# Kernel tuning notes

Hardware: AMD Instinct MI355X
Metric: run time of the kernel (lower is better)

## Reference

```python
import jax, jax.numpy as jnp
import numpy as np

B, N, M, D = 4, 4096, 4096, 64


def setup_inputs() -> dict:
    key = jax.random.key(0)
    kx, ky = jax.random.split(key)
    x = jax.random.normal(kx, (B, N, D), dtype=jnp.float32)
    y = jax.random.normal(ky, (B, M, D), dtype=jnp.float32)
    return {"x": x, "y": y}


def reference(x, y):
    # SparseMatmul3D forward: batched x @ y^T -> [B, N, M]
    return jnp.einsum("bnd,bmd->bnm", x, y)
```

## Files before the change

kernel.cpp:

```cpp
#include <hip/hip_runtime.h>


#define BATCH 4
#define NN 4096
#define MM 4096
#define DD 64

typedef __attribute__((ext_vector_type(8))) short bf16x8;
typedef __attribute__((ext_vector_type(4))) float f32x4;

__device__ __forceinline__ unsigned short f2bf(float f) {
    unsigned u = __builtin_bit_cast(unsigned, f);
    u += 0x7FFFu + ((u >> 16) & 1u);
    return (unsigned short)(u >> 16);
}

__device__ __forceinline__ bf16x8 cvt8(f32x4 v0, f32x4 v1) {
    bf16x8 r;
    r[0] = (short)f2bf(v0[0]); r[1] = (short)f2bf(v0[1]);
    r[2] = (short)f2bf(v0[2]); r[3] = (short)f2bf(v0[3]);
    r[4] = (short)f2bf(v1[0]); r[5] = (short)f2bf(v1[1]);
    r[6] = (short)f2bf(v1[2]); r[7] = (short)f2bf(v1[3]);
    return r;
}

__device__ __forceinline__ void stage_panel(const float* __restrict__ src,
                                            short* __restrict__ dst, int t) {
#pragma unroll
    for (int u = 0; u < 4; ++u) {
        const int f = u * 4096 + t * 8;
        f32x4 v0 = *reinterpret_cast<const f32x4*>(src + f);
        f32x4 v1 = *reinterpret_cast<const f32x4*>(src + f + 4);
        const int r  = (u << 6) + (t >> 3);
        const int un = (t & 7) ^ (r & 7);
        *reinterpret_cast<bf16x8*>(&dst[r * 64 + un * 8]) = cvt8(v0, v1);
    }
}

__global__ __launch_bounds__(512, 4) void
SparseMatmul3D_36155034698289_kernel(const float* __restrict__ x,
                                     const float* __restrict__ y,
                                     float* __restrict__ out) {
    const int bid = blockIdx.x;
    const int mc  = bid & 15;
    const int nt  = (bid >> 4) & 15;
    const int b   = bid >> 8;
    const int n0  = nt * 256;
    const int m0  = mc * 256;

    const int tid   = threadIdx.x;
    const int w     = tid >> 6;
    const int lane  = tid & 63;
    const int row16 = lane & 15;
    const int kgrp  = lane >> 4;
    const int wr    = w >> 1;
    const int wcp   = (w & 1) * 2;
    const int nloc  = wr * 64;

    __shared__ short xs[256 * 64];
    __shared__ short ys[256 * 64];

    stage_panel(x + (size_t)b * NN * DD + (size_t)n0 * DD, xs, tid);
    stage_panel(y + (size_t)b * MM * DD + (size_t)m0 * DD, ys, tid);
    __syncthreads();

    float* __restrict__ ob = out + (size_t)b * NN * MM;

#pragma unroll
    for (int tt = 0; tt < 2; ++tt) {
        const int mloc = (wcp + tt) * 64;

        f32x4 acc[4][4];
#pragma unroll
        for (int i = 0; i < 4; ++i)
#pragma unroll
            for (int j = 0; j < 4; ++j)
                acc[i][j] = (f32x4){0.f, 0.f, 0.f, 0.f};

#pragma unroll
        for (int i = 0; i < 4; ++i) {
            const int ra = mloc + i * 16 + row16;
            const bf16x8 a0 = *reinterpret_cast<const bf16x8*>(
                &ys[ra * 64 + ((kgrp       ^ (ra & 7)) * 8)]);
            const bf16x8 a1 = *reinterpret_cast<const bf16x8*>(
                &ys[ra * 64 + (((4 | kgrp) ^ (ra & 7)) * 8)]);
#pragma unroll
            for (int j = 0; j < 4; ++j) {
                const int rb = nloc + j * 16 + row16;
                const bf16x8 b0 = *reinterpret_cast<const bf16x8*>(
                    &xs[rb * 64 + ((kgrp       ^ (rb & 7)) * 8)]);
                const bf16x8 b1 = *reinterpret_cast<const bf16x8*>(
                    &xs[rb * 64 + (((4 | kgrp) ^ (rb & 7)) * 8)]);
                acc[i][j] = __builtin_amdgcn_mfma_f32_16x16x32_bf16(
                    a0, b0, acc[i][j], 0, 0, 0);
                acc[i][j] = __builtin_amdgcn_mfma_f32_16x16x32_bf16(
                    a1, b1, acc[i][j], 0, 0, 0);
            }
        }

#pragma unroll
        for (int j = 0; j < 4; ++j) {
            float* orow = ob + (size_t)(n0 + nloc + j * 16 + row16) * MM;
#pragma unroll
            for (int i = 0; i < 4; ++i)
                *reinterpret_cast<f32x4*>(
                    orow + m0 + mloc + i * 16 + kgrp * 4) = acc[i][j];
        }
    }
}

extern "C" void kernel_launch(void* const* d_in, const int* in_sizes, int n_in,
                              void* d_out, int out_size, void* d_ws, size_t ws_size,
                              hipStream_t stream) {
    const float* x = (const float*)d_in[0];
    const float* y = (const float*)d_in[1];
    float* out = (float*)d_out;

    dim3 grid(1024);
    dim3 block(512);
    SparseMatmul3D_36155034698289_kernel<<<grid, block, 0, stream>>>(x, y, out);
}
```

Baseline: 57.50 us.

## Pre-convert inputs to swizzled bf16 in workspace before matmul kernel

Adds a prepass kernel that converts x and y from fp32 to bf16 once and writes them already swizzled into a workspace buffer. The main kernel then copies bf16 panels straight into shared memory, so each block reads half the bytes and skips the per-block conversion that was repeated 16 times per panel. This costs an extra kernel launch and a workspace round trip, and keeps the old direct path as a fallback when the workspace is too small.

```diff
diff --git a/kernel.cpp b/kernel.cpp
--- a/kernel.cpp
+++ b/kernel.cpp
@@ -24,47 +24,35 @@
     return r;
 }
 
-__device__ __forceinline__ void stage_panel(const float* __restrict__ src,
-                                            short* __restrict__ dst, int t) {
-#pragma unroll
-    for (int u = 0; u < 4; ++u) {
-        const int f = u * 4096 + t * 8;
-        f32x4 v0 = *reinterpret_cast<const f32x4*>(src + f);
-        f32x4 v1 = *reinterpret_cast<const f32x4*>(src + f + 4);
-        const int r  = (u << 6) + (t >> 3);
-        const int un = (t & 7) ^ (r & 7);
-        *reinterpret_cast<bf16x8*>(&dst[r * 64 + un * 8]) = cvt8(v0, v1);
+__global__ __launch_bounds__(256) void
+preswz_kernel(const float* __restrict__ x, const float* __restrict__ y,
+              short* __restrict__ xscr, short* __restrict__ yscr) {
+    const int t = blockIdx.x * 256 + threadIdx.x;
+    const int R = t >> 3;
+    const int u = t & 7;
+    const int dst = R * 64 + ((u ^ (R & 7)) << 3);
+    {
+        const float* p = x + (size_t)t * 8;
+        f32x4 v0 = *reinterpret_cast<const f32x4*>(p);
+        f32x4 v1 = *reinterpret_cast<const f32x4*>(p + 4);
+        *reinterpret_cast<bf16x8*>(&xscr[dst]) = cvt8(v0, v1);
+    }
+    {
+        const float* p = y + (size_t)t * 8;
+        f32x4 v0 = *reinterpret_cast<const f32x4*>(p);
+        f32x4 v1 = *reinterpret_cast<const f32x4*>(p + 4);
+        *reinterpret_cast<bf16x8*>(&yscr[dst]) = cvt8(v0, v1);
     }
 }
 
-__global__ __launch_bounds__(512, 4) void
-SparseMatmul3D_36155034698289_kernel(const float* __restrict__ x,
-                                     const float* __restrict__ y,
-                                     float* __restrict__ out) {
-    const int bid = blockIdx.x;
-    const int mc  = bid & 15;
-    const int nt  = (bid >> 4) & 15;
-    const int b   = bid >> 8;
-    const int n0  = nt * 256;
-    const int m0  = mc * 256;
-
-    const int tid   = threadIdx.x;
-    const int w     = tid >> 6;
-    const int lane  = tid & 63;
+__device__ __forceinline__ void
+compute_and_store(const short* __restrict__ xs, const short* __restrict__ ys,
+                  float* __restrict__ ob, int n0, int m0, int w, int lane) {
     const int row16 = lane & 15;
     const int kgrp  = lane >> 4;
     const int wr    = w >> 1;
     const int wcp   = (w & 1) * 2;
     const int nloc  = wr * 64;
-
-    __shared__ short xs[256 * 64];
-    __shared__ short ys[256 * 64];
-
-    stage_panel(x + (size_t)b * NN * DD + (size_t)n0 * DD, xs, tid);
-    stage_panel(y + (size_t)b * MM * DD + (size_t)m0 * DD, ys, tid);
-    __syncthreads();
-
-    float* __restrict__ ob = out + (size_t)b * NN * MM;
 
 #pragma unroll
     for (int tt = 0; tt < 2; ++tt) {
@@ -100,13 +88,88 @@
 
 #pragma unroll
         for (int j = 0; j < 4; ++j) {
-            float* orow = ob + (size_t)(n0 + nloc + j * 16 + row16) * MM;
+            float* orow = ob + (size_t)(nloc + j * 16 + row16) * MM;
 #pragma unroll
             for (int i = 0; i < 4; ++i)
                 *reinterpret_cast<f32x4*>(
                     orow + m0 + mloc + i * 16 + kgrp * 4) = acc[i][j];
         }
     }
+}
+
+__global__ __launch_bounds__(512, 4) void
+SparseMatmul3D_36155034698289_kernel(const short* __restrict__ xscr,
+                                     const short* __restrict__ yscr,
+                                     float* __restrict__ out) {
+    const int bid = blockIdx.x;
+    const int mc  = bid & 15;
+    const int nt  = (bid >> 4) & 15;
+    const int b   = bid >> 8;
+    const int n0  = nt * 256;
+    const int m0  = mc * 256;
+
+    const int tid  = threadIdx.x;
+    const int w    = tid >> 6;
+    const int lane = tid & 63;
+
+    __shared__ short xs[256 * 64];
+    __shared__ short ys[256 * 64];
+
+    {
+        const bf16x8* xsrc = reinterpret_cast<const bf16x8*>(
+            xscr + (size_t)(b * NN + n0) * DD);
+        const bf16x8* ysrc = reinterpret_cast<const bf16x8*>(
+            yscr + (size_t)(b * MM + m0) * DD);
+        bf16x8* xdst = reinterpret_cast<bf16x8*>(xs);
+        bf16x8* ydst = reinterpret_cast<bf16x8*>(ys);
+#pragma unroll
+        for (int u = 0; u < 4; ++u) {
+            xdst[u * 512 + tid] = xsrc[u * 512 + tid];
+            ydst[u * 512 + tid] = ysrc[u * 512 + tid];
+        }
+    }
+    __syncthreads();
+
+    compute_and_store(xs, ys, out + (size_t)b * NN * MM + (size_t)n0 * MM,
+                      n0, m0, w, lane);
+}
+
+__device__ __forceinline__ void stage_panel(const float* __restrict__ src,
+                                            short* __restrict__ dst, int t) {
+#pragma unroll
+    for (int u = 0; u < 4; ++u) {
+        const int f = u * 4096 + t * 8;
+        f32x4 v0 = *reinterpret_cast<const f32x4*>(src + f);
+        f32x4 v1 = *reinterpret_cast<const f32x4*>(src + f + 4);
+        const int r  = (u << 6) + (t >> 3);
+        const int un = (t & 7) ^ (r & 7);
+        *reinterpret_cast<bf16x8*>(&dst[r * 64 + un * 8]) = cvt8(v0, v1);
+    }
+}
+
+__global__ __launch_bounds__(512, 4) void
+sparse_mm_direct_kernel(const float* __restrict__ x, const float* __restrict__ y,
+                        float* __restrict__ out) {
+    const int bid = blockIdx.x;
+    const int mc  = bid & 15;
+    const int nt  = (bid >> 4) & 15;
+    const int b   = bid >> 8;
+    const int n0  = nt * 256;
+    const int m0  = mc * 256;
+
+    const int tid  = threadIdx.x;
+    const int w    = tid >> 6;
+    const int lane = tid & 63;
+
+    __shared__ short xs[256 * 64];
+    __shared__ short ys[256 * 64];
+
+    stage_panel(x + (size_t)b * NN * DD + (size_t)n0 * DD, xs, tid);
+    stage_panel(y + (size_t)b * MM * DD + (size_t)m0 * DD, ys, tid);
+    __syncthreads();
+
+    compute_and_store(xs, ys, out + (size_t)b * NN * MM + (size_t)n0 * MM,
+                      n0, m0, w, lane);
 }
 
 extern "C" void kernel_launch(void* const* d_in, const int* in_sizes, int n_in,
@@ -116,7 +179,13 @@
     const float* y = (const float*)d_in[1];
     float* out = (float*)d_out;
 
-    dim3 grid(1024);
-    dim3 block(512);
-    SparseMatmul3D_36155034698289_kernel<<<grid, block, 0, stream>>>(x, y, out);
+    if (ws_size >= (size_t)4 * 1024 * 1024) {
+        short* xscr = (short*)d_ws;
+        short* yscr = (short*)d_ws + (size_t)BATCH * NN * DD;
+        preswz_kernel<<<dim3(512), dim3(256), 0, stream>>>(x, y, xscr, yscr);
+        SparseMatmul3D_36155034698289_kernel<<<dim3(1024), dim3(512), 0, stream>>>(
+            xscr, yscr, out);
+    } else {
+        sparse_mm_direct_kernel<<<dim3(1024), dim3(512), 0, stream>>>(x, y, out);
+    }
 }
```

Result: slower. 58.86 us (+2.4%).
